# Performance work log

Measured on AMD Instinct MI355X. Metric: run time of the kernel, lower is better.

## Reference

```python
import jax, jax.numpy as jnp
import numpy as np

D_MODEL = 1024
NUM_HEADS = 16
D_K = D_MODEL // NUM_HEADS


def setup_inputs() -> dict:
    key = jax.random.key(0)
    ks = jax.random.split(key, 11)
    B, T = 4, 2048
    s = 1.0 / np.sqrt(D_MODEL)
    return {
        'query': jax.random.normal(ks[0], (B, T, D_MODEL), jnp.float32),
        'key': jax.random.normal(ks[1], (B, T, D_MODEL), jnp.float32),
        'value': jax.random.normal(ks[2], (B, T, D_MODEL), jnp.float32),
        'Wq': jax.random.normal(ks[3], (D_MODEL, D_MODEL), jnp.float32) * s,
        'bq': jnp.zeros((D_MODEL,), jnp.float32),
        'Wk': jax.random.normal(ks[4], (D_MODEL, D_MODEL), jnp.float32) * s,
        'bk': jnp.zeros((D_MODEL,), jnp.float32),
        'Wv': jax.random.normal(ks[5], (D_MODEL, D_MODEL), jnp.float32) * s,
        'bv': jnp.zeros((D_MODEL,), jnp.float32),
        'Wo': jax.random.normal(ks[6], (D_MODEL, D_MODEL), jnp.float32) * s,
        'bo': jnp.zeros((D_MODEL,), jnp.float32),
    }


def reference(query, key, value, Wq, bq, Wk, bk, Wv, bv, Wo, bo):
    B, Tq, _ = query.shape
    Tk = key.shape[1]
    # projections (torch Linear: x @ W.T + b)
    q = (query @ Wq.T + bq).reshape(B, Tq, NUM_HEADS, D_K).transpose(0, 2, 1, 3)
    k = (key @ Wk.T + bk).reshape(B, Tk, NUM_HEADS, D_K).transpose(0, 2, 1, 3)
    v = (value @ Wv.T + bv).reshape(B, Tk, NUM_HEADS, D_K).transpose(0, 2, 1, 3)
    scale = 1.0 / jnp.sqrt(jnp.asarray(D_K, q.dtype))
    scores = jnp.einsum('bhqd,bhkd->bhqk', q, k) * scale  # [B,H,Tq,Tk]
    attn = jax.nn.softmax(scores, axis=-1)
    out = jnp.einsum('bhqk,bhkd->bhqd', attn, v)
    out = out.transpose(0, 2, 1, 3).reshape(B, Tq, D_MODEL)
    return out @ Wo.T + bo
```

## Files before the change

### kernel.cpp

```cpp
#include <hip/hip_runtime.h>

typedef unsigned short u16;
typedef unsigned int u32;
typedef __attribute__((ext_vector_type(8))) short bf16x8;
typedef __attribute__((ext_vector_type(4))) float f32x4;

__device__ inline u16 f2bf(float x) {
  union { float f; unsigned u; } v; v.f = x;
  unsigned r = v.u + 0x7fffu + ((v.u >> 16) & 1u);
  return (u16)(r >> 16);
}

__device__ inline u32 packbf2(float p0, float p1) {
  return __builtin_amdgcn_perm(__float_as_uint(p1), __float_as_uint(p0), 0x07060302u);
}

__device__ inline void gload16(const void* g, void* l) {
  __builtin_amdgcn_global_load_lds(
      (const __attribute__((address_space(1))) unsigned int*)g,
      (__attribute__((address_space(3))) unsigned int*)l,
      16, 0, 0);
}

__global__ void cvt_bf16_multi(const float* __restrict__ s0, const float* __restrict__ s1,
                               const float* __restrict__ s2, const float* __restrict__ s3,
                               u16* __restrict__ d0, u16* __restrict__ d1,
                               u16* __restrict__ d2, u16* __restrict__ d3, int n4) {
  int i = blockIdx.x * blockDim.x + threadIdx.x;
  if (i >= n4) return;
  int t = blockIdx.y;
  const float* src = (t == 0) ? s0 : (t == 1) ? s1 : (t == 2) ? s2 : s3;
  u16* dst = (t == 0) ? d0 : (t == 1) ? d1 : (t == 2) ? d2 : d3;
  float4 v = ((const float4*)src)[i];
  ushort4 o;
  o.x = f2bf(v.x); o.y = f2bf(v.y); o.z = f2bf(v.z); o.w = f2bf(v.w);
  ((ushort4*)dst)[i] = o;
}

template<int MODE>
__global__ __launch_bounds__(256, 2) void gemm_bt(
    const u16* __restrict__ A, const u16* __restrict__ W,
    const float* __restrict__ bias, void* __restrict__ Cout)
{
  constexpr int N = 1024, K = 1024, BK = 32;
  __shared__ __align__(16) u16 As[128 * BK];
  __shared__ __align__(16) u16 Bs[128 * BK];
  const int tid = threadIdx.x;
  const int wave = tid >> 6, lane = tid & 63;
  const int quad = lane >> 4, l16 = lane & 15;
  const int m0 = blockIdx.y * 128, n0 = blockIdx.x * 128;

  const int sA = wave * 2;
  const int srow = lane >> 2;
  const int skcol = (lane & 3) * 8;
  const int mloc = sA * 16 + srow;
  const int arow = (MODE == 1) ? ((mloc & 7) * 16 + (mloc >> 3)) : mloc;
  const int astep = (MODE == 1) ? 2 : 16;
  const u16* ag = A + (size_t)(m0 + arow) * K + skcol;
  const u16* bg = W + (size_t)(n0 + mloc) * K + skcol;
  u16* asl0 = As + sA * 512;  u16* asl1 = As + sA * 512 + 512;
  u16* bsl0 = Bs + sA * 512;  u16* bsl1 = Bs + sA * 512 + 512;

  const int wm = (wave >> 1) * 64, wn = (wave & 1) * 64;
  f32x4 acc[4][4] = {};

  for (int kt = 0; kt < K / BK; ++kt) {
    gload16(ag, asl0);
    gload16(ag + (size_t)astep * K, asl1);
    gload16(bg, bsl0);
    gload16(bg + 16 * K, bsl1);
    ag += BK; bg += BK;
    __syncthreads();
    bf16x8 af[4], bf[4];
#pragma unroll
    for (int mi = 0; mi < 4; ++mi)
      af[mi] = *(const bf16x8*)(As + (wm + mi * 16 + l16) * BK + quad * 8);
#pragma unroll
    for (int ni = 0; ni < 4; ++ni)
      bf[ni] = *(const bf16x8*)(Bs + (wn + ni * 16 + l16) * BK + quad * 8);
#pragma unroll
    for (int mi = 0; mi < 4; ++mi)
#pragma unroll
      for (int ni = 0; ni < 4; ++ni)
        acc[mi][ni] = __builtin_amdgcn_mfma_f32_16x16x32_bf16(af[mi], bf[ni], acc[mi][ni], 0, 0, 0);
    __syncthreads();
  }

#pragma unroll
  for (int ni = 0; ni < 4; ++ni) {
    const int col = n0 + wn + ni * 16 + l16;
    const float bv = bias[col];
#pragma unroll
    for (int mi = 0; mi < 4; ++mi) {
      const int mrow = m0 + wm + mi * 16 + quad * 4;
      f32x4 a = acc[mi][ni];
      if (MODE == 2) {
        float* C = (float*)Cout;
#pragma unroll
        for (int r = 0; r < 4; ++r)
          C[(size_t)(mrow + r) * N + col] = a[r] + bv;
      } else if (MODE == 0) {
        u16* C = (u16*)Cout;
#pragma unroll
        for (int r = 0; r < 4; ++r)
          C[(size_t)(mrow + r) * N + col] = f2bf(a[r] + bv);
      } else {
        u16* C = (u16*)Cout;
        const int bq = mrow >> 11, t = mrow & 2047;
        const int h = col >> 6, d = col & 63;
        ushort4 pk;
        pk.x = f2bf(a[0] + bv); pk.y = f2bf(a[1] + bv);
        pk.z = f2bf(a[2] + bv); pk.w = f2bf(a[3] + bv);
        *(ushort4*)(C + ((size_t)((bq * 16 + h) * 64 + d)) * 2048 + t) = pk;
      }
    }
  }
}

__global__ __launch_bounds__(512, 4) void flash_attn(
    const u16* __restrict__ Qp, const u16* __restrict__ Kp,
    const u16* __restrict__ Vt, u16* __restrict__ Ctx)
{
  constexpr int TQ = 2048, DM = 1024, DK = 64;
  constexpr int KP = 72;
  constexpr int VP = 136;
  __shared__ __align__(16) u16 Ks[128 * KP];
  __shared__ __align__(16) u16 Vts[64 * VP];
  __shared__ __align__(16) u16 Ps[8][16 * VP];

  const int bh = blockIdx.x, b = bh >> 4, h = bh & 15;
  const int qt = blockIdx.y;
  const int tid = threadIdx.x, wave = tid >> 6, lane = tid & 63;
  const int quad = lane >> 4, l16 = lane & 15;
  const int q0 = qt * 256 + wave * 32;

  bf16x8 qf[2][2];
#pragma unroll
  for (int mi = 0; mi < 2; ++mi)
#pragma unroll
    for (int ks = 0; ks < 2; ++ks)
      qf[mi][ks] = *(const bf16x8*)(Qp + (size_t)(b * TQ + q0 + mi * 16 + l16) * DM
                                       + h * DK + ks * 32 + quad * 8);

  f32x4 O[2][4] = {};
  f32x4 lsum[2] = {};
  const float CS = 0.18033688011112042f;
  const float C0 = 0.0028153f;

  bf16x8 onesv;
#pragma unroll
  for (int j = 0; j < 8; ++j) onesv[j] = (short)0x3F80;

  for (int kt = 0; kt < TQ / 128; ++kt) {
    const int k0 = kt * 128;
#pragma unroll
    for (int i = 0; i < 2; ++i) {
      int c = tid + i * 512;
      int row = c >> 3, seg = c & 7;
      *(float4*)(Ks + row * KP + seg * 8) =
          *(const float4*)(Kp + (size_t)(b * TQ + k0 + row) * DM + h * DK + seg * 8);
    }
#pragma unroll
    for (int i = 0; i < 2; ++i) {
      int c = tid + i * 512;
      int d = c >> 4, seg = c & 15;
      *(float4*)(Vts + d * VP + seg * 8) =
          *(const float4*)(Vt + ((size_t)(bh * DK + d)) * TQ + k0 + seg * 8);
    }
    __syncthreads();

#pragma unroll
    for (int mi = 0; mi < 2; ++mi) {
#pragma unroll
      for (int g = 0; g < 2; ++g) {
        f32x4 Sg[4];
#pragma unroll
        for (int cc = 0; cc < 4; ++cc) {
          const int c = g * 4 + cc;
          bf16x8 kf0 = *(const bf16x8*)(Ks + (c * 16 + l16) * KP + quad * 8);
          bf16x8 kf1 = *(const bf16x8*)(Ks + (c * 16 + l16) * KP + 32 + quad * 8);
          f32x4 z = {};
          z = __builtin_amdgcn_mfma_f32_16x16x32_bf16(qf[mi][0], kf0, z, 0, 0, 0);
          Sg[cc] = __builtin_amdgcn_mfma_f32_16x16x32_bf16(qf[mi][1], kf1, z, 0, 0, 0);
        }
#pragma unroll
        for (int r = 0; r < 4; ++r) {
          float e0 = exp2f(fmaf(Sg[0][r], CS, C0));
          float e1 = exp2f(fmaf(Sg[1][r], CS, C0));
          float e2 = exp2f(fmaf(Sg[2][r], CS, C0));
          float e3 = exp2f(fmaf(Sg[3][r], CS, C0));
          uint2 pk;
          pk.x = packbf2(e0, e1);
          pk.y = packbf2(e2, e3);
          *(uint2*)(&Ps[wave][(quad * 4 + r) * VP + l16 * 8 + g * 4]) = pk;
        }
      }
      bf16x8 pf[4];
#pragma unroll
      for (int ks = 0; ks < 4; ++ks)
        pf[ks] = *(const bf16x8*)(&Ps[wave][l16 * VP + ks * 32 + quad * 8]);
#pragma unroll
      for (int ks = 0; ks < 4; ++ks)
        lsum[mi] = __builtin_amdgcn_mfma_f32_16x16x32_bf16(pf[ks], onesv, lsum[mi], 0, 0, 0);
#pragma unroll
      for (int ks = 0; ks < 4; ++ks)
#pragma unroll
        for (int ni = 0; ni < 4; ++ni) {
          bf16x8 vf = *(const bf16x8*)(Vts + (ni * 16 + l16) * VP + ks * 32 + quad * 8);
          O[mi][ni] = __builtin_amdgcn_mfma_f32_16x16x32_bf16(pf[ks], vf, O[mi][ni], 0, 0, 0);
        }
    }
    __syncthreads();
  }

#pragma unroll
  for (int mi = 0; mi < 2; ++mi)
#pragma unroll
    for (int r = 0; r < 4; ++r) {
      const float inv = 1.0f / lsum[mi][r];
      const int q = q0 + mi * 16 + quad * 4 + r;
#pragma unroll
      for (int ni = 0; ni < 4; ++ni) {
        const int col = h * DK + ni * 16 + l16;
        Ctx[(size_t)(b * TQ + q) * DM + col] = f2bf(O[mi][ni][r] * inv);
      }
    }
}

extern "C" void kernel_launch(void* const* d_in, const int* in_sizes, int n_in,
                              void* d_out, int out_size, void* d_ws, size_t ws_size,
                              hipStream_t stream)
{
  (void)in_sizes; (void)n_in; (void)out_size; (void)ws_size;
  const float* query = (const float*)d_in[0];
  const float* key_  = (const float*)d_in[1];
  const float* value = (const float*)d_in[2];
  const float* Wq = (const float*)d_in[3];
  const float* bq = (const float*)d_in[4];
  const float* Wk = (const float*)d_in[5];
  const float* bk = (const float*)d_in[6];
  const float* Wv = (const float*)d_in[7];
  const float* bv = (const float*)d_in[8];
  const float* Wo = (const float*)d_in[9];
  const float* bo = (const float*)d_in[10];

  const size_t MT = (size_t)4 * 2048 * 1024;
  const size_t WT = (size_t)1024 * 1024;
  u16* ws  = (u16*)d_ws;
  u16* Xq  = ws;
  u16* Xk  = Xq + MT;
  u16* Xv  = Xk + MT;
  u16* Wqb = Xv + MT;
  u16* Wkb = Wqb + WT;
  u16* Wvb = Wkb + WT;
  u16* Wob = Wvb + WT;
  u16* Qp  = Wob + WT;
  u16* Kp  = Qp + MT;
  u16* Vt  = Kp + MT;
  u16* Ctx = Vt + MT;

  cvt_bf16_multi<<<dim3(8192, 3), 256, 0, stream>>>(
      query, key_, value, value, Xq, Xk, Xv, Xv, (int)(MT / 4));
  cvt_bf16_multi<<<dim3(1024, 4), 256, 0, stream>>>(
      Wq, Wk, Wv, Wo, Wqb, Wkb, Wvb, Wob, (int)(WT / 4));

  dim3 gg(8, 64);
  gemm_bt<0><<<gg, 256, 0, stream>>>(Xq, Wqb, bq, Qp);
  gemm_bt<0><<<gg, 256, 0, stream>>>(Xk, Wkb, bk, Kp);
  gemm_bt<1><<<gg, 256, 0, stream>>>(Xv, Wvb, bv, Vt);

  flash_attn<<<dim3(64, 8), 512, 0, stream>>>(Qp, Kp, Vt, Ctx);

  gemm_bt<2><<<gg, 256, 0, stream>>>(Ctx, Wob, bo, (float*)d_out);
}
```

Baseline: 391.1 us.

## Merge QKV projections into one launch, fold softmax scale, fragment-major LDS

The three Q/K/V projection GEMMs become a single launch with a 24-wide grid. Each block picks its input, bias and output segment from the column block, which relies on the workspace buffers and weights being contiguous. The softmax scale is folded into the Q projection epilogue, so the attention kernel can use raw hardware exp2 with no FMA and no constant offset. The GEMM and attention shared-memory tiles switch to a fragment-major layout: each lane reads 16 contiguous bytes indexed by lane, which is meant to avoid bank conflicts. The attention kernel also loads K/V tiles with async global-to-LDS loads, and GEMM occupancy is raised to 3 blocks per SM; the trade-off is slightly different rounding because Q is scaled before bf16 conversion.

Result: slower. 406.4 us (+3.9%).

```diff
diff --git a/kernel.cpp b/kernel.cpp
--- a/kernel.cpp
+++ b/kernel.cpp
@@ -37,31 +37,36 @@
   ((ushort4*)dst)[i] = o;
 }
 
+#define CS_SCALE 0.18033688011112042f
+
 template<int MODE>
-__global__ __launch_bounds__(256, 2) void gemm_bt(
+__global__ __launch_bounds__(256, 3) void gemm_bt(
     const u16* __restrict__ A, const u16* __restrict__ W,
-    const float* __restrict__ bias, void* __restrict__ Cout)
+    const float* __restrict__ b0, const float* __restrict__ b1,
+    const float* __restrict__ b2,
+    void* __restrict__ o0, void* __restrict__ o1, void* __restrict__ o2)
 {
-  constexpr int N = 1024, K = 1024, BK = 32;
+  constexpr int K = 1024, BK = 32;
   __shared__ __align__(16) u16 As[128 * BK];
   __shared__ __align__(16) u16 Bs[128 * BK];
   const int tid = threadIdx.x;
   const int wave = tid >> 6, lane = tid & 63;
   const int quad = lane >> 4, l16 = lane & 15;
   const int m0 = blockIdx.y * 128, n0 = blockIdx.x * 128;
-
-  const int sA = wave * 2;
-  const int srow = lane >> 2;
-  const int skcol = (lane & 3) * 8;
-  const int mloc = sA * 16 + srow;
-  const int arow = (MODE == 1) ? ((mloc & 7) * 16 + (mloc >> 3)) : mloc;
-  const int astep = (MODE == 1) ? 2 : 16;
-  const u16* ag = A + (size_t)(m0 + arow) * K + skcol;
-  const u16* bg = W + (size_t)(n0 + mloc) * K + skcol;
-  u16* asl0 = As + sA * 512;  u16* asl1 = As + sA * 512 + 512;
-  u16* bsl0 = Bs + sA * 512;  u16* bsl1 = Bs + sA * 512 + 512;
-
-  const int wm = (wave >> 1) * 64, wn = (wave & 1) * 64;
+  const int seg = (MODE == 0) ? (n0 >> 10) : 0;
+  const u16* Aseg = (MODE == 0) ? (A + (size_t)seg * 8192 * 1024) : A;
+
+  const int s0 = wave * 2;
+  const int mloc0 = s0 * 16 + l16;
+  const bool permA = (MODE == 0) && (seg == 2);
+  const int arow0 = permA ? ((mloc0 & 7) * 16 + (mloc0 >> 3)) : mloc0;
+  const int astep = permA ? 2 : 16;
+  const u16* ag = Aseg + (size_t)(m0 + arow0) * K + quad * 8;
+  const u16* bg = W + (size_t)(n0 + mloc0) * K + quad * 8;
+  u16* asl0 = As + s0 * 512;  u16* asl1 = As + s0 * 512 + 512;
+  u16* bsl0 = Bs + s0 * 512;  u16* bsl1 = Bs + s0 * 512 + 512;
+
+  const int ga = (wave >> 1) * 4, gb = (wave & 1) * 4;
   f32x4 acc[4][4] = {};
 
   for (int kt = 0; kt < K / BK; ++kt) {
@@ -74,10 +79,10 @@
     bf16x8 af[4], bf[4];
 #pragma unroll
     for (int mi = 0; mi < 4; ++mi)
-      af[mi] = *(const bf16x8*)(As + (wm + mi * 16 + l16) * BK + quad * 8);
+      af[mi] = *(const bf16x8*)(As + (ga + mi) * 512 + lane * 8);
 #pragma unroll
     for (int ni = 0; ni < 4; ++ni)
-      bf[ni] = *(const bf16x8*)(Bs + (wn + ni * 16 + l16) * BK + quad * 8);
+      bf[ni] = *(const bf16x8*)(Bs + (gb + ni) * 512 + lane * 8);
 #pragma unroll
     for (int mi = 0; mi < 4; ++mi)
 #pragma unroll
@@ -86,32 +91,35 @@
     __syncthreads();
   }
 
+  const float scl = (MODE == 0 && seg == 0) ? CS_SCALE : 1.0f;
+  const float* bias = (MODE == 2) ? b0 : (seg == 0 ? b0 : (seg == 1 ? b1 : b2));
 #pragma unroll
   for (int ni = 0; ni < 4; ++ni) {
-    const int col = n0 + wn + ni * 16 + l16;
-    const float bv = bias[col];
+    const int col_g = n0 + gb * 16 + ni * 16 + l16;
+    const int col_l = col_g & 1023;
+    const float bv = bias[col_l];
 #pragma unroll
     for (int mi = 0; mi < 4; ++mi) {
-      const int mrow = m0 + wm + mi * 16 + quad * 4;
+      const int mrow = m0 + ga * 16 + mi * 16 + quad * 4;
       f32x4 a = acc[mi][ni];
       if (MODE == 2) {
-        float* C = (float*)Cout;
+        float* C = (float*)o0;
 #pragma unroll
         for (int r = 0; r < 4; ++r)
-          C[(size_t)(mrow + r) * N + col] = a[r] + bv;
-      } else if (MODE == 0) {
-        u16* C = (u16*)Cout;
-#pragma unroll
-        for (int r = 0; r < 4; ++r)
-          C[(size_t)(mrow + r) * N + col] = f2bf(a[r] + bv);
-      } else {
-        u16* C = (u16*)Cout;
+          C[(size_t)(mrow + r) * 1024 + col_l] = a[r] + bv;
+      } else if (seg == 2) {
+        u16* C = (u16*)o2;
         const int bq = mrow >> 11, t = mrow & 2047;
-        const int h = col >> 6, d = col & 63;
+        const int h = col_l >> 6, d = col_l & 63;
         ushort4 pk;
         pk.x = f2bf(a[0] + bv); pk.y = f2bf(a[1] + bv);
         pk.z = f2bf(a[2] + bv); pk.w = f2bf(a[3] + bv);
         *(ushort4*)(C + ((size_t)((bq * 16 + h) * 64 + d)) * 2048 + t) = pk;
+      } else {
+        u16* C = (u16*)(seg == 0 ? o0 : o1);
+#pragma unroll
+        for (int r = 0; r < 4; ++r)
+          C[(size_t)(mrow + r) * 1024 + col_l] = f2bf((a[r] + bv) * scl);
       }
     }
   }
@@ -122,10 +130,9 @@
     const u16* __restrict__ Vt, u16* __restrict__ Ctx)
 {
   constexpr int TQ = 2048, DM = 1024, DK = 64;
-  constexpr int KP = 72;
   constexpr int VP = 136;
-  __shared__ __align__(16) u16 Ks[128 * KP];
-  __shared__ __align__(16) u16 Vts[64 * VP];
+  __shared__ __align__(16) u16 Ks[128 * DK];
+  __shared__ __align__(16) u16 Vts[DK * 128];
   __shared__ __align__(16) u16 Ps[8][16 * VP];
 
   const int bh = blockIdx.x, b = bh >> 4, h = bh & 15;
@@ -144,28 +151,23 @@
 
   f32x4 O[2][4] = {};
   f32x4 lsum[2] = {};
-  const float CS = 0.18033688011112042f;
-  const float C0 = 0.0028153f;
 
   bf16x8 onesv;
 #pragma unroll
   for (int j = 0; j < 8; ++j) onesv[j] = (short)0x3F80;
+
+  const int ki0 = wave * 2;
 
   for (int kt = 0; kt < TQ / 128; ++kt) {
     const int k0 = kt * 128;
 #pragma unroll
     for (int i = 0; i < 2; ++i) {
-      int c = tid + i * 512;
-      int row = c >> 3, seg = c & 7;
-      *(float4*)(Ks + row * KP + seg * 8) =
-          *(const float4*)(Kp + (size_t)(b * TQ + k0 + row) * DM + h * DK + seg * 8);
-    }
-#pragma unroll
-    for (int i = 0; i < 2; ++i) {
-      int c = tid + i * 512;
-      int d = c >> 4, seg = c & 15;
-      *(float4*)(Vts + d * VP + seg * 8) =
-          *(const float4*)(Vt + ((size_t)(bh * DK + d)) * TQ + k0 + seg * 8);
+      const int ki = ki0 + i, c = ki >> 1, kp = ki & 1;
+      gload16(Kp + (size_t)(b * TQ + k0 + c * 16 + l16) * DM + h * DK + (kp * 4 + quad) * 8,
+              Ks + ki * 512);
+      const int vks = ki >> 2, vni = ki & 3;
+      gload16(Vt + ((size_t)(bh * DK + vni * 16 + l16)) * TQ + k0 + vks * 32 + quad * 8,
+              Vts + ki * 512);
     }
     __syncthreads();
 
@@ -177,18 +179,18 @@
 #pragma unroll
         for (int cc = 0; cc < 4; ++cc) {
           const int c = g * 4 + cc;
-          bf16x8 kf0 = *(const bf16x8*)(Ks + (c * 16 + l16) * KP + quad * 8);
-          bf16x8 kf1 = *(const bf16x8*)(Ks + (c * 16 + l16) * KP + 32 + quad * 8);
+          bf16x8 kf0 = *(const bf16x8*)(Ks + (c * 2 + 0) * 512 + lane * 8);
+          bf16x8 kf1 = *(const bf16x8*)(Ks + (c * 2 + 1) * 512 + lane * 8);
           f32x4 z = {};
           z = __builtin_amdgcn_mfma_f32_16x16x32_bf16(qf[mi][0], kf0, z, 0, 0, 0);
           Sg[cc] = __builtin_amdgcn_mfma_f32_16x16x32_bf16(qf[mi][1], kf1, z, 0, 0, 0);
         }
 #pragma unroll
         for (int r = 0; r < 4; ++r) {
-          float e0 = exp2f(fmaf(Sg[0][r], CS, C0));
-          float e1 = exp2f(fmaf(Sg[1][r], CS, C0));
-          float e2 = exp2f(fmaf(Sg[2][r], CS, C0));
-          float e3 = exp2f(fmaf(Sg[3][r], CS, C0));
+          float e0 = __builtin_amdgcn_exp2f(Sg[0][r]);
+          float e1 = __builtin_amdgcn_exp2f(Sg[1][r]);
+          float e2 = __builtin_amdgcn_exp2f(Sg[2][r]);
+          float e3 = __builtin_amdgcn_exp2f(Sg[3][r]);
           uint2 pk;
           pk.x = packbf2(e0, e1);
           pk.y = packbf2(e2, e3);
@@ -206,7 +208,7 @@
       for (int ks = 0; ks < 4; ++ks)
 #pragma unroll
         for (int ni = 0; ni < 4; ++ni) {
-          bf16x8 vf = *(const bf16x8*)(Vts + (ni * 16 + l16) * VP + ks * 32 + quad * 8);
+          bf16x8 vf = *(const bf16x8*)(Vts + (ks * 4 + ni) * 512 + lane * 8);
           O[mi][ni] = __builtin_amdgcn_mfma_f32_16x16x32_bf16(pf[ks], vf, O[mi][ni], 0, 0, 0);
         }
     }
@@ -264,12 +266,11 @@
   cvt_bf16_multi<<<dim3(1024, 4), 256, 0, stream>>>(
       Wq, Wk, Wv, Wo, Wqb, Wkb, Wvb, Wob, (int)(WT / 4));
 
-  dim3 gg(8, 64);
-  gemm_bt<0><<<gg, 256, 0, stream>>>(Xq, Wqb, bq, Qp);
-  gemm_bt<0><<<gg, 256, 0, stream>>>(Xk, Wkb, bk, Kp);
-  gemm_bt<1><<<gg, 256, 0, stream>>>(Xv, Wvb, bv, Vt);
+  gemm_bt<0><<<dim3(24, 64), 256, 0, stream>>>(
+      Xq, Wqb, bq, bk, bv, Qp, Kp, Vt);
 
   flash_attn<<<dim3(64, 8), 512, 0, stream>>>(Qp, Kp, Vt, Ctx);
 
-  gemm_bt<2><<<gg, 256, 0, stream>>>(Ctx, Wob, bo, (float*)d_out);
-}
+  gemm_bt<2><<<dim3(8, 64), 256, 0, stream>>>(
+      Ctx, Wob, bo, bo, bo, (float*)d_out, nullptr, nullptr);
+}
```
